# Kernel tuning notes

Measured on AMD Instinct MI355X. Metric: run time of the kernel, lower is better.

The kernel has to match this reference:

```python
import jax, jax.numpy as jnp
import numpy as np

N, IN_C, HID, H1, E, EP = 4096, 256, 128, 4, 131072, 131072
TH, TL, FF = 4, 2, 512  # transformer heads, layers, ffn dim
D = HID  # transformer d_model


def setup_inputs() -> dict:
    key = jax.random.key(0)
    ks = jax.random.split(key, 32)
    s = 0.05
    inp = {
        'features': jax.random.normal(ks[0], (N, IN_C), jnp.float32),
        'src': jax.random.randint(ks[1], (E,), 0, N),
        'dst': jax.random.randint(ks[2], (E,), 0, N),
        'psrc': jax.random.randint(ks[3], (EP,), 0, N),
        'pdst': jax.random.randint(ks[4], (EP,), 0, N),
        # GAT layer 1: in=256 -> heads=4, out=128
        'W1': jax.random.normal(ks[5], (H1 * HID, IN_C), jnp.float32) * s,
        'al1': jax.random.normal(ks[6], (H1, HID), jnp.float32) * s,
        'ar1': jax.random.normal(ks[7], (H1, HID), jnp.float32) * s,
        'b1': jnp.zeros((H1 * HID,), jnp.float32),
        # GAT layer 2: in=512 -> heads=1, out=128
        'W2': jax.random.normal(ks[8], (HID, H1 * HID), jnp.float32) * s,
        'al2': jax.random.normal(ks[9], (1, HID), jnp.float32) * s,
        'ar2': jax.random.normal(ks[10], (1, HID), jnp.float32) * s,
        'b2': jnp.zeros((HID,), jnp.float32),
        # Transformer encoder (TL layers, torch TransformerEncoderLayer post-norm, relu)
        'tw_qkv': jax.random.normal(ks[11], (TL, 3 * D, D), jnp.float32) * s,
        'tb_qkv': jnp.zeros((TL, 3 * D), jnp.float32),
        'tw_o': jax.random.normal(ks[12], (TL, D, D), jnp.float32) * s,
        'tb_o': jnp.zeros((TL, D), jnp.float32),
        'ln1_g': jnp.ones((TL, D), jnp.float32),
        'ln1_b': jnp.zeros((TL, D), jnp.float32),
        'tw_ff1': jax.random.normal(ks[13], (TL, FF, D), jnp.float32) * s,
        'tb_ff1': jnp.zeros((TL, FF), jnp.float32),
        'tw_ff2': jax.random.normal(ks[14], (TL, D, FF), jnp.float32) * s,
        'tb_ff2': jnp.zeros((TL, D), jnp.float32),
        'ln2_g': jnp.ones((TL, D), jnp.float32),
        'ln2_b': jnp.zeros((TL, D), jnp.float32),
        # decoder MLP
        'fc1_w': jax.random.normal(ks[15], (HID, 2 * HID), jnp.float32) * s,
        'fc1_b': jnp.zeros((HID,), jnp.float32),
        'fc2_w': jax.random.normal(ks[16], (1, HID), jnp.float32) * s,
        'fc2_b': jnp.zeros((1,), jnp.float32),
    }
    return inp


def _leaky(x):
    return jnp.where(x > 0, x, 0.2 * x)


def _gat(x, W, al, ar, b, src, dst, n):
    H, F = al.shape
    h = (x @ W.T).reshape(n, H, F)  # [N,H,F]
    el = jnp.sum(h * al[None], -1)  # [N,H]
    er = jnp.sum(h * ar[None], -1)
    e = _leaky(el[src] + er[dst])  # [E,H]
    m = jax.ops.segment_max(e, dst, num_segments=n)
    ex = jnp.exp(e - m[dst])
    ssum = jax.ops.segment_sum(ex, dst, num_segments=n)
    alpha = ex / ssum[dst]  # edge softmax over incoming edges of dst
    out = jax.ops.segment_sum(h[src] * alpha[:, :, None], dst, num_segments=n)
    return out + b.reshape(1, H, F)


def _ln(x, g, b):
    mu = jnp.mean(x, -1, keepdims=True)
    var = jnp.mean((x - mu) ** 2, -1, keepdims=True)
    return (x - mu) / jnp.sqrt(var + 1e-5) * g + b


def _encoder_layer(h, wqkv, bqkv, wo, bo, g1, b1, wf1, bf1, wf2, bf2, g2, b2):
    n, d = h.shape
    hd = d // TH
    qkv = h @ wqkv.T + bqkv
    q, k, v = jnp.split(qkv, 3, axis=-1)
    q = q.reshape(n, TH, hd)
    k = k.reshape(n, TH, hd)
    v = v.reshape(n, TH, hd)
    scores = jnp.einsum('qhd,khd->hqk', q, k) / jnp.sqrt(jnp.float32(hd))
    attn = jax.nn.softmax(scores, axis=-1)
    o = jnp.einsum('hqk,khd->qhd', attn, v).reshape(n, d) @ wo.T + bo
    h = _ln(h + o, g1, b1)
    ff = jax.nn.relu(h @ wf1.T + bf1) @ wf2.T + bf2
    return _ln(h + ff, g2, b2)


def reference(features, W1, al1, ar1, b1, W2, al2, ar2, b2,
              tw_qkv, tb_qkv, tw_o, tb_o, ln1_g, ln1_b,
              tw_ff1, tb_ff1, tw_ff2, tb_ff2, ln2_g, ln2_b,
              fc1_w, fc1_b, fc2_w, fc2_b, src, dst, psrc, pdst):
    n = features.shape[0]
    h = _gat(features, W1, al1, ar1, b1, src, dst, n)  # [N,4,128]
    h = jax.nn.relu(h.reshape(n, -1))                  # [N,512]
    h = _gat(h, W2, al2, ar2, b2, src, dst, n)[:, 0]   # [N,128]
    for i in range(TL):
        h = _encoder_layer(h, tw_qkv[i], tb_qkv[i], tw_o[i], tb_o[i],
                           ln1_g[i], ln1_b[i], tw_ff1[i], tb_ff1[i],
                           tw_ff2[i], tb_ff2[i], ln2_g[i], ln2_b[i])
    ef = jnp.concatenate([h[psrc], h[pdst]], axis=1)   # [EP,256]
    x = jax.nn.relu(ef @ fc1_w.T + fc1_b)
    return jax.nn.sigmoid(x @ fc2_w.T + fc2_b)         # [EP,1]
```

## Files before the change

kernel.cpp:

```cpp
#include <hip/hip_runtime.h>
#include <hip/hip_bf16.h>
#include <math.h>

#define NN   4096
#define INC  256
#define HIDF 128
#define H1H  4
#define DM   128
#define THD  4
#define FFD  512

typedef __attribute__((ext_vector_type(8))) short bf16x8;
typedef __attribute__((ext_vector_type(4))) float f32x4;

__device__ __forceinline__ float leaky(float x){ return x > 0.f ? x : 0.2f*x; }

__device__ __forceinline__ ushort f2b(float f){
  __hip_bfloat16 h = __float2bfloat16(f);
  return __builtin_bit_cast(ushort, h);
}
__device__ __forceinline__ unsigned pk2(float a, float b){
  return (unsigned)f2b(a) | ((unsigned)f2b(b) << 16);
}
__device__ __forceinline__ float b2f(unsigned u){ return __uint_as_float(u << 16); }
__device__ __forceinline__ float b2flo(unsigned u){ return __uint_as_float(u << 16); }
__device__ __forceinline__ float b2fhi(unsigned u){ return __uint_as_float(u & 0xffff0000u); }

__device__ __forceinline__ int kvperm(int kv){
  return (kv & ~31) | ((kv & 12) << 1) | ((kv >> 2) & 4) | (kv & 3);
}

template<bool BIAS, bool RELU, bool OUTBF, bool ABF>
__global__ __launch_bounds__(256) void gemm_mf(
    const void* __restrict__ Av, const ushort* __restrict__ Wb,
    const float* __restrict__ bias, void* __restrict__ Cv,
    int M, int N, int K, int ldw)
{
  __shared__ uint4 As4[512];
  __shared__ uint4 Bs4[512];
  int tid = threadIdx.x;
  int row0 = blockIdx.y * 64, col0 = blockIdx.x * 64;
  int wid = tid >> 6, lane = tid & 63;
  int wm = wid >> 1, wn = wid & 1;
  int ql = lane & 15, g = lane >> 4;
  const f32x4 z4 = {0.f,0.f,0.f,0.f};
  f32x4 acc[2][2] = {z4,z4,z4,z4};

  for (int k0 = 0; k0 < K; k0 += 64) {
    #pragma unroll
    for (int p = 0; p < 2; p++) {
      int idx = tid + p*256;
      int ko = idx & 7, mm = idx >> 3;
      if constexpr (ABF) {
        As4[ko*64 + mm] = *(const uint4*)((const ushort*)Av + (size_t)(row0 + mm)*K + k0 + ko*8);
      } else {
        const float* sa = (const float*)Av + (size_t)(row0 + mm)*K + k0 + ko*8;
        float4 a0 = *(const float4*)sa;
        float4 a1 = *(const float4*)(sa + 4);
        uint4 av;
        av.x = pk2(a0.x, a0.y); av.y = pk2(a0.z, a0.w);
        av.z = pk2(a1.x, a1.y); av.w = pk2(a1.z, a1.w);
        As4[ko*64 + mm] = av;
      }
      Bs4[ko*64 + mm] = *(const uint4*)(Wb + (size_t)(col0 + mm)*ldw + k0 + ko*8);
    }
    __syncthreads();
    #pragma unroll
    for (int kk = 0; kk < 2; kk++) {
      int ko = kk*4 + g;
      bf16x8 a0 = *((const bf16x8*)As4 + ko*64 + wm*32 + ql);
      bf16x8 a1 = *((const bf16x8*)As4 + ko*64 + wm*32 + 16 + ql);
      bf16x8 b0 = *((const bf16x8*)Bs4 + ko*64 + wn*32 + ql);
      bf16x8 b1 = *((const bf16x8*)Bs4 + ko*64 + wn*32 + 16 + ql);
      acc[0][0] = __builtin_amdgcn_mfma_f32_16x16x32_bf16(a0, b0, acc[0][0], 0,0,0);
      acc[0][1] = __builtin_amdgcn_mfma_f32_16x16x32_bf16(a0, b1, acc[0][1], 0,0,0);
      acc[1][0] = __builtin_amdgcn_mfma_f32_16x16x32_bf16(a1, b0, acc[1][0], 0,0,0);
      acc[1][1] = __builtin_amdgcn_mfma_f32_16x16x32_bf16(a1, b1, acc[1][1], 0,0,0);
    }
    __syncthreads();
  }
  float bvs[2] = {0.f, 0.f};
  if (BIAS) {
    bvs[0] = bias[col0 + wn*32 + ql];
    bvs[1] = bias[col0 + wn*32 + 16 + ql];
  }
  #pragma unroll
  for (int fm = 0; fm < 2; fm++)
    #pragma unroll
    for (int fn = 0; fn < 2; fn++) {
      int row = row0 + wm*32 + fm*16 + g*4;
      int col = col0 + wn*32 + fn*16 + ql;
      #pragma unroll
      for (int r = 0; r < 4; r++) {
        float v = acc[fm][fn][r];
        if (BIAS) v += bvs[fn];
        if (RELU) v = fmaxf(v, 0.f);
        if (OUTBF) ((ushort*)Cv)[(size_t)(row + r)*N + col] = f2b(v);
        else       ((float*)Cv)[(size_t)(row + r)*N + col] = v;
      }
    }
}

__global__ __launch_bounds__(256) void gemm_qkv(
    const ushort* __restrict__ Ab, const ushort* __restrict__ Wb,
    const float* __restrict__ bias,
    ushort* __restrict__ qb, ushort* __restrict__ kt, ushort* __restrict__ vt)
{
  __shared__ uint4 As4[512];
  __shared__ uint4 Bs4[512];
  int tid = threadIdx.x;
  int row0 = blockIdx.y * 64, col0 = blockIdx.x * 64;
  int wid = tid >> 6, lane = tid & 63;
  int wm = wid >> 1, wn = wid & 1;
  int ql = lane & 15, g = lane >> 4;
  const f32x4 z4 = {0.f,0.f,0.f,0.f};
  f32x4 acc[2][2] = {z4,z4,z4,z4};

  for (int k0 = 0; k0 < 128; k0 += 64) {
    #pragma unroll
    for (int p = 0; p < 2; p++) {
      int idx = tid + p*256;
      int ko = idx & 7, mm = idx >> 3;
      As4[ko*64 + mm] = *(const uint4*)(Ab + (size_t)(row0 + mm)*128 + k0 + ko*8);
      Bs4[ko*64 + mm] = *(const uint4*)(Wb + (size_t)(col0 + mm)*128 + k0 + ko*8);
    }
    __syncthreads();
    #pragma unroll
    for (int kk = 0; kk < 2; kk++) {
      int ko = kk*4 + g;
      bf16x8 a0 = *((const bf16x8*)As4 + ko*64 + wm*32 + ql);
      bf16x8 a1 = *((const bf16x8*)As4 + ko*64 + wm*32 + 16 + ql);
      bf16x8 b0 = *((const bf16x8*)Bs4 + ko*64 + wn*32 + ql);
      bf16x8 b1 = *((const bf16x8*)Bs4 + ko*64 + wn*32 + 16 + ql);
      acc[0][0] = __builtin_amdgcn_mfma_f32_16x16x32_bf16(a0, b0, acc[0][0], 0,0,0);
      acc[0][1] = __builtin_amdgcn_mfma_f32_16x16x32_bf16(a0, b1, acc[0][1], 0,0,0);
      acc[1][0] = __builtin_amdgcn_mfma_f32_16x16x32_bf16(a1, b0, acc[1][0], 0,0,0);
      acc[1][1] = __builtin_amdgcn_mfma_f32_16x16x32_bf16(a1, b1, acc[1][1], 0,0,0);
    }
    __syncthreads();
  }
  float bvs[2];
  bvs[0] = bias[col0 + wn*32 + ql];
  bvs[1] = bias[col0 + wn*32 + 16 + ql];
  #pragma unroll
  for (int fm = 0; fm < 2; fm++)
    #pragma unroll
    for (int fn = 0; fn < 2; fn++) {
      int row = row0 + wm*32 + fm*16 + g*4;
      int col = col0 + wn*32 + fn*16 + ql;
      #pragma unroll
      for (int r = 0; r < 4; r++) {
        float v = acc[fm][fn][r] + bvs[fn];
        int kv = row + r;
        if (col < 128) {
          qb[(size_t)kv*128 + col] = f2b(v * 0.25505654708f);
        } else if (col < 256) {
          int hh = (col - 128) >> 5, d = (col - 128) & 31;
          kt[(size_t)hh*131072 + (size_t)kv*32 + d] = f2b(v);
        } else {
          int hh = (col - 256) >> 5, d = (col - 256) & 31;
          vt[(size_t)hh*131072 + (size_t)(kv >> 5)*1024 + (d >> 4)*512
             + (d & 15)*32 + kvperm(kv & 31)] = f2b(v);
        }
      }
    }
}

__global__ __launch_bounds__(256) void gemm_ln(
    const ushort* __restrict__ Ab, const ushort* __restrict__ Wb,
    const float* __restrict__ bias, ushort* __restrict__ h,
    const float* __restrict__ lng, const float* __restrict__ lnb, int K)
{
  __shared__ uint4 As4[128];
  __shared__ uint4 Bs4[1024];
  __shared__ float xs[16][132];
  int tid = threadIdx.x;
  int row0 = blockIdx.x * 16;
  int wv = tid >> 6, lane = tid & 63;
  int ql = lane & 15, g = lane >> 4;
  const f32x4 z4 = {0.f,0.f,0.f,0.f};
  f32x4 acc[2] = {z4, z4};

  for (int k0 = 0; k0 < K; k0 += 64) {
    if (tid < 128) {
      int ko = tid & 7, mm = tid >> 3;
      As4[ko*16 + mm] = *(const uint4*)(Ab + (size_t)(row0 + mm)*K + k0 + ko*8);
    }
    #pragma unroll
    for (int p = 0; p < 4; p++) {
      int idx = tid + p*256;
      int ko = idx & 7, nn = idx >> 3;
      Bs4[ko*128 + nn] = *(const uint4*)(Wb + (size_t)nn*K + k0 + ko*8);
    }
    __syncthreads();
    #pragma unroll
    for (int kk = 0; kk < 2; kk++) {
      int ko = kk*4 + g;
      bf16x8 a = *((const bf16x8*)As4 + ko*16 + ql);
      #pragma unroll
      for (int fn = 0; fn < 2; fn++) {
        bf16x8 b = *((const bf16x8*)Bs4 + ko*128 + wv*32 + fn*16 + ql);
        acc[fn] = __builtin_amdgcn_mfma_f32_16x16x32_bf16(a, b, acc[fn], 0,0,0);
      }
    }
    __syncthreads();
  }
  #pragma unroll
  for (int fn = 0; fn < 2; fn++) {
    int col = wv*32 + fn*16 + ql;
    float bv = bias[col];
    #pragma unroll
    for (int r = 0; r < 4; r++) xs[g*4 + r][col] = acc[fn][r] + bv;
  }
  __syncthreads();
  int rl = tid >> 4, cl = tid & 15, c0 = cl * 8;
  ushort* hrow = h + (size_t)(row0 + rl)*128;
  uint4 rv = *(const uint4*)(hrow + c0);
  float x[8];
  x[0] = xs[rl][c0+0] + b2flo(rv.x); x[1] = xs[rl][c0+1] + b2fhi(rv.x);
  x[2] = xs[rl][c0+2] + b2flo(rv.y); x[3] = xs[rl][c0+3] + b2fhi(rv.y);
  x[4] = xs[rl][c0+4] + b2flo(rv.z); x[5] = xs[rl][c0+5] + b2fhi(rv.z);
  x[6] = xs[rl][c0+6] + b2flo(rv.w); x[7] = xs[rl][c0+7] + b2fhi(rv.w);
  float s1 = 0.f, s2 = 0.f;
  #pragma unroll
  for (int i = 0; i < 8; i++) { s1 += x[i]; s2 += x[i]*x[i]; }
  #pragma unroll
  for (int st = 1; st < 16; st <<= 1) {
    s1 += __shfl_xor(s1, st); s2 += __shfl_xor(s2, st);
  }
  float mean = s1 * (1.f/128.f);
  float var  = s2 * (1.f/128.f) - mean*mean;
  float rstd = rsqrtf(var + 1e-5f);
  float o[8];
  #pragma unroll
  for (int i = 0; i < 8; i += 4) {
    float4 g4 = *(const float4*)(lng + c0 + i);
    float4 b4 = *(const float4*)(lnb + c0 + i);
    o[i+0] = (x[i+0]-mean)*rstd*g4.x + b4.x;
    o[i+1] = (x[i+1]-mean)*rstd*g4.y + b4.y;
    o[i+2] = (x[i+2]-mean)*rstd*g4.z + b4.z;
    o[i+3] = (x[i+3]-mean)*rstd*g4.w + b4.w;
  }
  uint4 ov; ov.x = pk2(o[0],o[1]); ov.y = pk2(o[2],o[3]);
  ov.z = pk2(o[4],o[5]); ov.w = pk2(o[6],o[7]);
  *(uint4*)(hrow + c0) = ov;
}

__global__ __launch_bounds__(256) void cvt_weights(
    const float* __restrict__ W1, const float* __restrict__ W2,
    const float* __restrict__ qkv, const float* __restrict__ o,
    const float* __restrict__ ff1, const float* __restrict__ ff2,
    const float* __restrict__ fc1, const float* __restrict__ fc1b,
    ushort* __restrict__ out, float* __restrict__ bias256)
{
  if (blockIdx.x == 608) {
    int t = threadIdx.x;
    bias256[t] = (t < 128) ? fc1b[t] : 0.f;
    return;
  }
  int i4 = (blockIdx.x*256 + threadIdx.x) * 4;
  const float* s; int loc;
  size_t dst = i4;
  if      (i4 < 131072) { s = W1;  loc = i4; }
  else if (i4 < 196608) { s = W2;  loc = i4 - 131072; }
  else if (i4 < 294912) { s = qkv; loc = i4 - 196608; }
  else if (i4 < 327680) { s = o;   loc = i4 - 294912; }
  else if (i4 < 458752) { s = ff1; loc = i4 - 327680; }
  else if (i4 < 589824) { s = ff2; loc = i4 - 458752; }
  else {
    s = fc1; loc = i4 - 589824;
    int j = loc >> 8, k2 = loc & 255;
    dst = 589824 + ((k2 >= 128) ? 16384 : 0) + j*128 + (k2 & 127);
  }
  float4 v = *(const float4*)(s + loc);
  uint2 w; w.x = pk2(v.x, v.y); w.y = pk2(v.z, v.w);
  *(uint2*)(out + dst) = w;
}

__global__ __launch_bounds__(256) void cvt_feat(
    const float* __restrict__ f, ushort* __restrict__ o)
{
  int i = (blockIdx.x * 256 + threadIdx.x) * 4;
  float4 v = *(const float4*)(f + i);
  uint2 w; w.x = pk2(v.x, v.y); w.y = pk2(v.z, v.w);
  *(uint2*)(o + i) = w;
}

__global__ void count_kernel(const int* __restrict__ dst, int* __restrict__ deg, int E) {
  int e = blockIdx.x * blockDim.x + threadIdx.x;
  if (e < E) atomicAdd(&deg[dst[e]], 1);
}
__global__ __launch_bounds__(1024) void scan_kernel(
    const int* __restrict__ deg, int* __restrict__ rowstart, int* __restrict__ cursor)
{
  __shared__ int sdata[1024];
  int t = threadIdx.x;
  int base = t * 4;
  int v0 = deg[base], v1 = deg[base+1], v2 = deg[base+2], v3 = deg[base+3];
  int tot = v0 + v1 + v2 + v3;
  sdata[t] = tot;
  __syncthreads();
  for (int off = 1; off < 1024; off <<= 1) {
    int x = (t >= off) ? sdata[t - off] : 0;
    __syncthreads();
    sdata[t] += x;
    __syncthreads();
  }
  int run = sdata[t] - tot;
  rowstart[base]   = run; cursor[base]   = run; run += v0;
  rowstart[base+1] = run; cursor[base+1] = run; run += v1;
  rowstart[base+2] = run; cursor[base+2] = run; run += v2;
  rowstart[base+3] = run; cursor[base+3] = run; run += v3;
  if (t == 1023) rowstart[4096] = run;
}
__global__ void fill_kernel(const int* __restrict__ src, const int* __restrict__ dst,
                            int* __restrict__ cursor, int* __restrict__ nbr, int E) {
  int e = blockIdx.x * blockDim.x + threadIdx.x;
  if (e < E) {
    int p = atomicAdd(&cursor[dst[e]], 1);
    nbr[p] = src[e];
  }
}

template<int H>
__global__ __launch_bounds__(256) void elr_kernel(
    const ushort* __restrict__ hmat, const float* __restrict__ al,
    const float* __restrict__ ar, float* __restrict__ el, float* __restrict__ er)
{
  int w = threadIdx.x >> 6, lane = threadIdx.x & 63;
  int n = blockIdx.x * 4 + w;
  if constexpr (H == 4) {
    int hh = lane >> 4, f0 = (lane & 15) * 8;
    bf16x8 hv = *(const bf16x8*)(hmat + (size_t)n*512 + hh*128 + f0);
    float4 a0 = *(const float4*)(al + hh*128 + f0);
    float4 a1 = *(const float4*)(al + hh*128 + f0 + 4);
    float4 r0 = *(const float4*)(ar + hh*128 + f0);
    float4 r1 = *(const float4*)(ar + hh*128 + f0 + 4);
    float x[8];
    #pragma unroll
    for (int i = 0; i < 8; i++) x[i] = b2f((ushort)hv[i]);
    float e1 = x[0]*a0.x + x[1]*a0.y + x[2]*a0.z + x[3]*a0.w
             + x[4]*a1.x + x[5]*a1.y + x[6]*a1.z + x[7]*a1.w;
    float e2 = x[0]*r0.x + x[1]*r0.y + x[2]*r0.z + x[3]*r0.w
             + x[4]*r1.x + x[5]*r1.y + x[6]*r1.z + x[7]*r1.w;
    #pragma unroll
    for (int s = 1; s < 16; s <<= 1) { e1 += __shfl_xor(e1, s); e2 += __shfl_xor(e2, s); }
    if ((lane & 15) == 0) { el[n*4 + hh] = e1; er[n*4 + hh] = e2; }
  } else {
    int f0 = lane * 2;
    unsigned u = *(const unsigned*)(hmat + (size_t)n*128 + f0);
    float x0 = b2flo(u), x1 = b2fhi(u);
    float2 av = *(const float2*)(al + f0);
    float2 rv = *(const float2*)(ar + f0);
    float e1 = x0*av.x + x1*av.y;
    float e2 = x0*rv.x + x1*rv.y;
    #pragma unroll
    for (int s = 1; s < 64; s <<= 1) { e1 += __shfl_xor(e1, s); e2 += __shfl_xor(e2, s); }
    if (lane == 0) { el[n] = e1; er[n] = e2; }
  }
}

__global__ __launch_bounds__(256) void gat_agg4(
    const ushort* __restrict__ hsrc, const float* __restrict__ el, const float* __restrict__ er,
    const int* __restrict__ rowstart, const int* __restrict__ nbr,
    const float* __restrict__ bias, ushort* __restrict__ out)
{
  __shared__ float s_alpha[4][256][4];
  __shared__ int   s_nbr[4][256];
  int wv = threadIdx.x >> 6, lane = threadIdx.x & 63;
  int n = blockIdx.x * 4 + wv;
  int e0 = rowstart[n];
  int deg = rowstart[n+1] - e0;
  float4 ern = *(const float4*)(er + (size_t)n*4);
  int hh = lane >> 4;
  float acc[8] = {};
  if (deg > 0 && deg <= 256) {
    float se0=0.f, se1=0.f, se2=0.f, se3=0.f;
    for (int i = lane; i < deg; i += 64) {
      int s = nbr[e0 + i];
      s_nbr[wv][i] = s;
      float4 ev = *(const float4*)(el + (size_t)s*4);
      float p0 = __expf(leaky(ev.x + ern.x));
      float p1 = __expf(leaky(ev.y + ern.y));
      float p2 = __expf(leaky(ev.z + ern.z));
      float p3 = __expf(leaky(ev.w + ern.w));
      s_alpha[wv][i][0] = p0; s_alpha[wv][i][1] = p1;
      s_alpha[wv][i][2] = p2; s_alpha[wv][i][3] = p3;
      se0 += p0; se1 += p1; se2 += p2; se3 += p3;
    }
    #pragma unroll
    for (int st = 1; st < 64; st <<= 1) {
      se0 += __shfl_xor(se0, st); se1 += __shfl_xor(se1, st);
      se2 += __shfl_xor(se2, st); se3 += __shfl_xor(se3, st);
    }
    float si = 1.f / ((hh == 0) ? se0 : (hh == 1) ? se1 : (hh == 2) ? se2 : se3);
    #pragma unroll 4
    for (int i = 0; i < deg; i++) {
      float a = s_alpha[wv][i][hh] * si;
      int s = s_nbr[wv][i];
      uint4 hv = *(const uint4*)(hsrc + (size_t)s*512 + lane*8);
      acc[0] += a * b2flo(hv.x); acc[1] += a * b2fhi(hv.x);
      acc[2] += a * b2flo(hv.y); acc[3] += a * b2fhi(hv.y);
      acc[4] += a * b2flo(hv.z); acc[5] += a * b2fhi(hv.z);
      acc[6] += a * b2flo(hv.w); acc[7] += a * b2fhi(hv.w);
    }
  } else if (deg > 0) {
    float se0=0.f, se1=0.f, se2=0.f, se3=0.f;
    for (int i = lane; i < deg; i += 64) {
      int s = nbr[e0 + i];
      float4 ev = *(const float4*)(el + (size_t)s*4);
      se0 += __expf(leaky(ev.x + ern.x));
      se1 += __expf(leaky(ev.y + ern.y));
      se2 += __expf(leaky(ev.z + ern.z));
      se3 += __expf(leaky(ev.w + ern.w));
    }
    #pragma unroll
    for (int st = 1; st < 64; st <<= 1) {
      se0 += __shfl_xor(se0, st); se1 += __shfl_xor(se1, st);
      se2 += __shfl_xor(se2, st); se3 += __shfl_xor(se3, st);
    }
    float si0 = 1.f/se0, si1 = 1.f/se1, si2 = 1.f/se2, si3 = 1.f/se3;
    for (int c = 0; c < deg; c += 256) {
      int cn = min(256, deg - c);
      for (int i = lane; i < cn; i += 64) {
        int s = nbr[e0 + c + i];
        s_nbr[wv][i] = s;
        float4 ev = *(const float4*)(el + (size_t)s*4);
        s_alpha[wv][i][0] = __expf(leaky(ev.x + ern.x)) * si0;
        s_alpha[wv][i][1] = __expf(leaky(ev.y + ern.y)) * si1;
        s_alpha[wv][i][2] = __expf(leaky(ev.z + ern.z)) * si2;
        s_alpha[wv][i][3] = __expf(leaky(ev.w + ern.w)) * si3;
      }
      #pragma unroll 4
      for (int i = 0; i < cn; i++) {
        float a = s_alpha[wv][i][hh];
        int s = s_nbr[wv][i];
        uint4 hv = *(const uint4*)(hsrc + (size_t)s*512 + lane*8);
        acc[0] += a * b2flo(hv.x); acc[1] += a * b2fhi(hv.x);
        acc[2] += a * b2flo(hv.y); acc[3] += a * b2fhi(hv.y);
        acc[4] += a * b2flo(hv.z); acc[5] += a * b2fhi(hv.z);
        acc[6] += a * b2flo(hv.w); acc[7] += a * b2fhi(hv.w);
      }
    }
  }
  const float* bp = bias + lane*8;
  float4 b0 = *(const float4*)(bp);
  float4 b1 = *(const float4*)(bp + 4);
  float v0 = fmaxf(acc[0]+b0.x, 0.f), v1 = fmaxf(acc[1]+b0.y, 0.f);
  float v2 = fmaxf(acc[2]+b0.z, 0.f), v3 = fmaxf(acc[3]+b0.w, 0.f);
  float v4 = fmaxf(acc[4]+b1.x, 0.f), v5 = fmaxf(acc[5]+b1.y, 0.f);
  float v6 = fmaxf(acc[6]+b1.z, 0.f), v7 = fmaxf(acc[7]+b1.w, 0.f);
  uint4 ov; ov.x = pk2(v0,v1); ov.y = pk2(v2,v3); ov.z = pk2(v4,v5); ov.w = pk2(v6,v7);
  *(uint4*)(out + (size_t)n*512 + lane*8) = ov;
}

__global__ __launch_bounds__(256) void gat_agg1(
    const ushort* __restrict__ hsrc, const float* __restrict__ el, const float* __restrict__ er,
    const int* __restrict__ rowstart, const int* __restrict__ nbr,
    const float* __restrict__ bias, ushort* __restrict__ out)
{
  __shared__ float s_alpha[4][256];
  __shared__ int   s_nbr[4][256];
  int wv = threadIdx.x >> 6, lane = threadIdx.x & 63;
  int n = blockIdx.x * 4 + wv;
  int e0 = rowstart[n];
  int deg = rowstart[n+1] - e0;
  float ern = er[n];
  float a0 = 0.f, a1 = 0.f;
  if (deg > 0 && deg <= 256) {
    float se = 0.f;
    for (int i = lane; i < deg; i += 64) {
      int s = nbr[e0 + i];
      s_nbr[wv][i] = s;
      float p = __expf(leaky(el[s] + ern));
      s_alpha[wv][i] = p;
      se += p;
    }
    #pragma unroll
    for (int st = 1; st < 64; st <<= 1) se += __shfl_xor(se, st);
    float si = 1.f / se;
    #pragma unroll 4
    for (int i = 0; i < deg; i++) {
      float a = s_alpha[wv][i] * si;
      int s = s_nbr[wv][i];
      unsigned u = *(const unsigned*)(hsrc + (size_t)s*128 + lane*2);
      a0 += a * b2flo(u);
      a1 += a * b2fhi(u);
    }
  } else if (deg > 0) {
    float se = 0.f;
    for (int i = lane; i < deg; i += 64)
      se += __expf(leaky(el[nbr[e0 + i]] + ern));
    #pragma unroll
    for (int st = 1; st < 64; st <<= 1) se += __shfl_xor(se, st);
    float si = 1.f / se;
    for (int c = 0; c < deg; c += 256) {
      int cn = min(256, deg - c);
      for (int i = lane; i < cn; i += 64) {
        int s = nbr[e0 + c + i];
        s_nbr[wv][i] = s;
        s_alpha[wv][i] = __expf(leaky(el[s] + ern)) * si;
      }
      #pragma unroll 4
      for (int i = 0; i < cn; i++) {
        float a = s_alpha[wv][i];
        int s = s_nbr[wv][i];
        unsigned u = *(const unsigned*)(hsrc + (size_t)s*128 + lane*2);
        a0 += a * b2flo(u);
        a1 += a * b2fhi(u);
      }
    }
  }
  float v0 = a0 + bias[lane*2], v1 = a1 + bias[lane*2 + 1];
  *(unsigned*)(out + (size_t)n*128 + lane*2) = pk2(v0, v1);
}

#define LOADFRAGS(KF, VF, KV)                                              \
  {                                                                        \
    int _kv = (KV);                                                        \
    if (_kv < 512) {                                                       \
      const ushort* _kp = kptr + (size_t)_kv * 32;                         \
      const ushort* _vp = vptr + (size_t)_kv * 32;                         \
      KF[0] = *(const bf16x8*)(_kp);                                       \
      KF[1] = *(const bf16x8*)(_kp + 512);                                 \
      KF[2] = *(const bf16x8*)(_kp + 1024);                                \
      KF[3] = *(const bf16x8*)(_kp + 1536);                                \
      VF[0] = *(const bf16x8*)(_vp);                                       \
      VF[1] = *(const bf16x8*)(_vp + 1024);                                \
      VF[2] = *(const bf16x8*)(_vp + 512);                                 \
      VF[3] = *(const bf16x8*)(_vp + 1536);                                \
    }                                                                      \
  }

#define QPASS(QF, LS, OA, OB, KF, VF)                                      \
  {                                                                        \
    f32x4 st0 = __builtin_amdgcn_mfma_f32_16x16x32_bf16(KF[0], QF, z4, 0, 0, 0); \
    f32x4 st1 = __builtin_amdgcn_mfma_f32_16x16x32_bf16(KF[1], QF, z4, 0, 0, 0); \
    f32x4 st2 = __builtin_amdgcn_mfma_f32_16x16x32_bf16(KF[2], QF, z4, 0, 0, 0); \
    f32x4 st3 = __builtin_amdgcn_mfma_f32_16x16x32_bf16(KF[3], QF, z4, 0, 0, 0); \
    float pvv[16];                                                         \
    _Pragma("unroll")                                                      \
    for (int i = 0; i < 4; i++) {                                          \
      pvv[i] = st0[i]; pvv[4+i] = st1[i]; pvv[8+i] = st2[i]; pvv[12+i] = st3[i]; \
    }                                                                      \
    _Pragma("unroll")                                                      \
    for (int i = 0; i < 16; i++) { pvv[i] = exp2f(pvv[i]); LS += pvv[i]; } \
    bf16x8 pf0 = { (short)f2b(pvv[0]),  (short)f2b(pvv[1]),  (short)f2b(pvv[2]),  (short)f2b(pvv[3]),   \
                   (short)f2b(pvv[4]),  (short)f2b(pvv[5]),  (short)f2b(pvv[6]),  (short)f2b(pvv[7]) }; \
    bf16x8 pf1 = { (short)f2b(pvv[8]),  (short)f2b(pvv[9]),  (short)f2b(pvv[10]), (short)f2b(pvv[11]),  \
                   (short)f2b(pvv[12]), (short)f2b(pvv[13]), (short)f2b(pvv[14]), (short)f2b(pvv[15]) };\
    OA = __builtin_amdgcn_mfma_f32_16x16x32_bf16(VF[0], pf0, OA, 0, 0, 0); \
    OA = __builtin_amdgcn_mfma_f32_16x16x32_bf16(VF[1], pf1, OA, 0, 0, 0); \
    OB = __builtin_amdgcn_mfma_f32_16x16x32_bf16(VF[2], pf0, OB, 0, 0, 0); \
    OB = __builtin_amdgcn_mfma_f32_16x16x32_bf16(VF[3], pf1, OB, 0, 0, 0); \
  }

#define ATTN_BODY(KF, VF, KN, VN, KV)                                      \
  {                                                                        \
    LOADFRAGS(KN, VN, (KV) + 64);                                          \
    QPASS(qf0, ls0, o00, o01, KF, VF);                                     \
    QPASS(qf1, ls1, o10, o11, KF, VF);                                     \
  }

__global__ __launch_bounds__(512) void attn_mfma(
    const ushort* __restrict__ qb,
    const ushort* __restrict__ kt,
    const ushort* __restrict__ vt,
    ushort* __restrict__ attnout)
{
  int lane = threadIdx.x & 63;
  int w    = threadIdx.x >> 6;
  int head = blockIdx.x >> 7;
  int q0   = (blockIdx.x & 127) * 32;
  int ql = lane & 15;
  int g  = lane >> 4;
  const f32x4 z4 = {0.f, 0.f, 0.f, 0.f};
  int kvbase = w * 512;

  bf16x8 qf0 = *(const bf16x8*)(qb + (size_t)(q0 + ql)*128      + head*32 + g*8);
  bf16x8 qf1 = *(const bf16x8*)(qb + (size_t)(q0 + 16 + ql)*128 + head*32 + g*8);
  const ushort* kptr = kt + (size_t)head*131072 + (size_t)kvbase*32 + ql*32 + g*8;
  const ushort* vptr = vt + (size_t)head*131072 + (size_t)kvbase*32 + ql*32 + g*8;

  float ls0 = 0.f, ls1 = 0.f;
  f32x4 o00 = z4, o01 = z4, o10 = z4, o11 = z4;

  bf16x8 kfA[4], vfA[4], kfB[4], vfB[4];
  LOADFRAGS(kfA, vfA, 0);
  for (int kv0 = 0; kv0 < 512; kv0 += 128) {
    ATTN_BODY(kfA, vfA, kfB, vfB, kv0);
    ATTN_BODY(kfB, vfB, kfA, vfA, kv0 + 64);
  }

  ls0 += __shfl_xor(ls0, 16); ls0 += __shfl_xor(ls0, 32);
  ls1 += __shfl_xor(ls1, 16); ls1 += __shfl_xor(ls1, 32);

  __shared__ float so[8][32][36];
  __shared__ float sl[8][32];
  if (g == 0) { sl[w][ql] = ls0; sl[w][16 + ql] = ls1; }
  #pragma unroll
  for (int r = 0; r < 4; r++) {
    so[w][ql][g*4 + r]           = o00[r];
    so[w][ql][16 + g*4 + r]      = o01[r];
    so[w][16 + ql][g*4 + r]      = o10[r];
    so[w][16 + ql][16 + g*4 + r] = o11[r];
  }
  __syncthreads();
  int q  = threadIdx.x >> 4;
  int d0 = (threadIdx.x & 15) * 2;
  float L = 0.f, O0 = 0.f, O1 = 0.f;
  #pragma unroll
  for (int w2 = 0; w2 < 8; w2++) {
    L  += sl[w2][q];
    O0 += so[w2][q][d0];
    O1 += so[w2][q][d0+1];
  }
  float rl = 1.f / L;
  *(unsigned*)(attnout + (size_t)(q0 + q)*128 + head*32 + d0) = pk2(O0*rl, O1*rl);
}

__global__ __launch_bounds__(256) void pair_kernel(
    const ushort* __restrict__ ABp,
    const int* __restrict__ ps, const int* __restrict__ pd,
    const float* __restrict__ fc2w, const float* __restrict__ fc2b,
    float* __restrict__ out, int EP)
{
  int gw = (blockIdx.x * blockDim.x + threadIdx.x) >> 6;
  int lane = threadIdx.x & 63;
  int nw = (gridDim.x * blockDim.x) >> 6;
  float w0 = fc2w[2*lane], w1 = fc2w[2*lane + 1];
  float bb = fc2b[0];
  for (int p = gw*2; p < EP; p += nw*2) {
    int sA = ps[p], dA = pd[p];
    bool hasB = (p + 1 < EP);
    int sB = hasB ? ps[p+1] : sA;
    int dB = hasB ? pd[p+1] : dA;
    unsigned avA = *(const unsigned*)(ABp + (size_t)sA*256 + 2*lane);
    unsigned bvA = *(const unsigned*)(ABp + (size_t)dA*256 + 128 + 2*lane);
    unsigned avB = *(const unsigned*)(ABp + (size_t)sB*256 + 2*lane);
    unsigned bvB = *(const unsigned*)(ABp + (size_t)dB*256 + 128 + 2*lane);
    float accA = fmaxf(b2flo(avA) + b2flo(bvA), 0.f)*w0
               + fmaxf(b2fhi(avA) + b2fhi(bvA), 0.f)*w1;
    float accB = fmaxf(b2flo(avB) + b2flo(bvB), 0.f)*w0
               + fmaxf(b2fhi(avB) + b2fhi(bvB), 0.f)*w1;
    #pragma unroll
    for (int off = 32; off > 0; off >>= 1) {
      accA += __shfl_down(accA, off);
      accB += __shfl_down(accB, off);
    }
    if (lane == 0) {
      out[p] = 1.f / (1.f + __expf(-(accA + bb)));
      if (hasB) out[p+1] = 1.f / (1.f + __expf(-(accB + bb)));
    }
  }
}

extern "C" void kernel_launch(void* const* d_in, const int* in_sizes, int n_in,
                              void* d_out, int out_size, void* d_ws, size_t ws_size,
                              hipStream_t stream)
{
  const float* features = (const float*)d_in[0];
  const int*   src      = (const int*)d_in[1];
  const int*   dst      = (const int*)d_in[2];
  const int*   psrc     = (const int*)d_in[3];
  const int*   pdst     = (const int*)d_in[4];
  const float* W1   = (const float*)d_in[5];
  const float* al1  = (const float*)d_in[6];
  const float* ar1  = (const float*)d_in[7];
  const float* b1   = (const float*)d_in[8];
  const float* W2   = (const float*)d_in[9];
  const float* al2  = (const float*)d_in[10];
  const float* ar2  = (const float*)d_in[11];
  const float* b2   = (const float*)d_in[12];
  const float* tw_qkv = (const float*)d_in[13];
  const float* tb_qkv = (const float*)d_in[14];
  const float* tw_o   = (const float*)d_in[15];
  const float* tb_o   = (const float*)d_in[16];
  const float* ln1_g  = (const float*)d_in[17];
  const float* ln1_b  = (const float*)d_in[18];
  const float* tw_ff1 = (const float*)d_in[19];
  const float* tb_ff1 = (const float*)d_in[20];
  const float* tw_ff2 = (const float*)d_in[21];
  const float* tb_ff2 = (const float*)d_in[22];
  const float* ln2_g  = (const float*)d_in[23];
  const float* ln2_b  = (const float*)d_in[24];
  const float* fc1_w  = (const float*)d_in[25];
  const float* fc1_b  = (const float*)d_in[26];
  const float* fc2_w  = (const float*)d_in[27];
  const float* fc2_b  = (const float*)d_in[28];
  int E  = in_sizes[1];
  int EP = in_sizes[3];

  float* ws = (float*)d_ws;
  size_t off = 0;
  auto alloc = [&](size_t n) { float* p = ws + off; off += n; return p; };
  ushort* hb    = (ushort*)alloc((size_t)NN * 64);
  ushort* featb = (ushort*)alloc((size_t)NN * 128);
  ushort* h1b   = (ushort*)alloc((size_t)NN * 256);
  ushort* h2b   = (ushort*)alloc((size_t)NN * 256);
  ushort* bigb  = (ushort*)alloc((size_t)NN * 256);
  ushort* hgb   = (ushort*)alloc((size_t)NN * 64);
  ushort* qb    = (ushort*)alloc((size_t)NN * 64);
  ushort* attnb = (ushort*)alloc((size_t)NN * 64);
  ushort* kt    = (ushort*)alloc((size_t)NN * 64);
  ushort* vt    = (ushort*)alloc((size_t)NN * 64);
  ushort* wbf   = (ushort*)alloc(622592/2);
  ushort* ABp   = (ushort*)alloc((size_t)NN * 128);
  float*  bias256 = alloc(256);
  float*  el1   = alloc((size_t)NN * 4);
  float*  er1   = alloc((size_t)NN * 4);
  float*  el2   = alloc((size_t)NN);
  float*  er2   = alloc((size_t)NN);
  int* ibase    = (int*)(ws + off);
  int* deg      = ibase;
  int* rowstart = ibase + 4096;
  int* cursor   = rowstart + 4097;
  int* nbr      = cursor + 4096;

  const size_t oW1 = 0, oW2 = 131072, oQKV = 196608, oO = 294912,
               oFF1 = 327680, oFF2 = 458752, oFC1 = 589824;

  cvt_weights<<<609, 256, 0, stream>>>(W1, W2, tw_qkv, tw_o, tw_ff1, tw_ff2,
                                       fc1_w, fc1_b, wbf, bias256);
  cvt_feat<<<1024, 256, 0, stream>>>(features, featb);

  hipMemsetAsync(deg, 0, 4096 * sizeof(int), stream);
  count_kernel<<<(E + 255)/256, 256, 0, stream>>>(dst, deg, E);
  scan_kernel<<<1, 1024, 0, stream>>>(deg, rowstart, cursor);
  fill_kernel<<<(E + 255)/256, 256, 0, stream>>>(src, dst, cursor, nbr, E);

  gemm_mf<false,false,true,true><<<dim3(8, 64), 256, 0, stream>>>(
      featb, wbf + oW1, nullptr, h1b, NN, 512, 256, 256);
  elr_kernel<4><<<1024, 256, 0, stream>>>(h1b, al1, ar1, el1, er1);
  gat_agg4<<<1024, 256, 0, stream>>>(h1b, el1, er1, rowstart, nbr, b1, h2b);

  gemm_mf<false,false,true,true><<<dim3(2, 64), 256, 0, stream>>>(
      h2b, wbf + oW2, nullptr, hgb, NN, 128, 512, 512);
  elr_kernel<1><<<1024, 256, 0, stream>>>(hgb, al2, ar2, el2, er2);
  gat_agg1<<<1024, 256, 0, stream>>>(hgb, el2, er2, rowstart, nbr, b2, hb);

  for (int l = 0; l < 2; l++) {
    gemm_qkv<<<dim3(6, 64), 256, 0, stream>>>(
        hb, wbf + oQKV + (size_t)l*49152, tb_qkv + l*384, qb, kt, vt);
    attn_mfma<<<512, 512, 0, stream>>>(qb, kt, vt, attnb);
    gemm_ln<<<256, 256, 0, stream>>>(
        attnb, wbf + oO + (size_t)l*16384, tb_o + l*128, hb,
        ln1_g + l*128, ln1_b + l*128, 128);
    gemm_mf<true,true,true,true><<<dim3(8, 64), 256, 0, stream>>>(
        hb, wbf + oFF1 + (size_t)l*65536, tb_ff1 + l*512, bigb, NN, 512, 128, 128);
    gemm_ln<<<256, 256, 0, stream>>>(
        bigb, wbf + oFF2 + (size_t)l*65536, tb_ff2 + l*128, hb,
        ln2_g + l*128, ln2_b + l*128, 512);
  }

  gemm_mf<true,false,true,true><<<dim3(4, 64), 256, 0, stream>>>(
      hb, wbf + oFC1, bias256, ABp, NN, 256, 128, 128);
  pair_kernel<<<1024, 256, 0, stream>>>(ABp, psrc, pdst, fc2_w, fc2_b, (float*)d_out, EP);
}
```

Before: 212.4 us.

## Fuse layer-2 GAT projection with attention logits; merge conversion kernels; widen pair batching

Adds a dedicated GEMM kernel for the second GAT projection that also computes the el/er attention logits in its epilogue from fp32 accumulators, removing a separate elr launch and a reread of the projected features. The weight and feature bf16 conversion kernels are merged into one launch. The pair decoder kernel now processes four pairs per wave iteration instead of two, to raise memory-level parallelism on the gathers. In exchange, the new GEMM uses 16-row tiles and reloads the full 128x64 weight tile per block, and el/er now come from fp32 values rather than bf16-rounded ones.

```diff
diff --git a/kernel.cpp b/kernel.cpp
--- a/kernel.cpp
+++ b/kernel.cpp
@@ -246,19 +246,97 @@
   *(uint4*)(hrow + c0) = ov;
 }
 
-__global__ __launch_bounds__(256) void cvt_weights(
+__global__ __launch_bounds__(256) void gemm_hg_elr(
+    const ushort* __restrict__ Ab, const ushort* __restrict__ Wb,
+    const float* __restrict__ al, const float* __restrict__ ar,
+    ushort* __restrict__ hg, float* __restrict__ el, float* __restrict__ er)
+{
+  __shared__ uint4 As4[128];
+  __shared__ uint4 Bs4[1024];
+  __shared__ float xs[16][132];
+  int tid = threadIdx.x;
+  int row0 = blockIdx.x * 16;
+  int wv = tid >> 6, lane = tid & 63;
+  int ql = lane & 15, g = lane >> 4;
+  const f32x4 z4 = {0.f,0.f,0.f,0.f};
+  f32x4 acc[2] = {z4, z4};
+
+  for (int k0 = 0; k0 < 512; k0 += 64) {
+    if (tid < 128) {
+      int ko = tid & 7, mm = tid >> 3;
+      As4[ko*16 + mm] = *(const uint4*)(Ab + (size_t)(row0 + mm)*512 + k0 + ko*8);
+    }
+    #pragma unroll
+    for (int p = 0; p < 4; p++) {
+      int idx = tid + p*256;
+      int ko = idx & 7, nn = idx >> 3;
+      Bs4[ko*128 + nn] = *(const uint4*)(Wb + (size_t)nn*512 + k0 + ko*8);
+    }
+    __syncthreads();
+    #pragma unroll
+    for (int kk = 0; kk < 2; kk++) {
+      int ko = kk*4 + g;
+      bf16x8 a = *((const bf16x8*)As4 + ko*16 + ql);
+      #pragma unroll
+      for (int fn = 0; fn < 2; fn++) {
+        bf16x8 b = *((const bf16x8*)Bs4 + ko*128 + wv*32 + fn*16 + ql);
+        acc[fn] = __builtin_amdgcn_mfma_f32_16x16x32_bf16(a, b, acc[fn], 0,0,0);
+      }
+    }
+    __syncthreads();
+  }
+  #pragma unroll
+  for (int fn = 0; fn < 2; fn++) {
+    int col = wv*32 + fn*16 + ql;
+    #pragma unroll
+    for (int r = 0; r < 4; r++) xs[g*4 + r][col] = acc[fn][r];
+  }
+  __syncthreads();
+  int rl = tid >> 4, cl = tid & 15, c0 = cl * 8;
+  float e1 = 0.f, e2 = 0.f;
+  float x[8];
+  #pragma unroll
+  for (int i = 0; i < 8; i += 4) {
+    float4 a4 = *(const float4*)(al + c0 + i);
+    float4 r4 = *(const float4*)(ar + c0 + i);
+    x[i+0] = xs[rl][c0+i+0]; x[i+1] = xs[rl][c0+i+1];
+    x[i+2] = xs[rl][c0+i+2]; x[i+3] = xs[rl][c0+i+3];
+    e1 += x[i+0]*a4.x + x[i+1]*a4.y + x[i+2]*a4.z + x[i+3]*a4.w;
+    e2 += x[i+0]*r4.x + x[i+1]*r4.y + x[i+2]*r4.z + x[i+3]*r4.w;
+  }
+  uint4 ov; ov.x = pk2(x[0],x[1]); ov.y = pk2(x[2],x[3]);
+  ov.z = pk2(x[4],x[5]); ov.w = pk2(x[6],x[7]);
+  *(uint4*)(hg + (size_t)(row0 + rl)*128 + c0) = ov;
+  #pragma unroll
+  for (int st = 1; st < 16; st <<= 1) {
+    e1 += __shfl_xor(e1, st); e2 += __shfl_xor(e2, st);
+  }
+  if (cl == 0) { el[row0 + rl] = e1; er[row0 + rl] = e2; }
+}
+
+__global__ __launch_bounds__(256) void cvt_all(
     const float* __restrict__ W1, const float* __restrict__ W2,
     const float* __restrict__ qkv, const float* __restrict__ o,
     const float* __restrict__ ff1, const float* __restrict__ ff2,
     const float* __restrict__ fc1, const float* __restrict__ fc1b,
-    ushort* __restrict__ out, float* __restrict__ bias256)
-{
-  if (blockIdx.x == 608) {
+    const float* __restrict__ feat,
+    ushort* __restrict__ out, float* __restrict__ bias256,
+    ushort* __restrict__ featb)
+{
+  int b = blockIdx.x;
+  if (b == 608) {
     int t = threadIdx.x;
     bias256[t] = (t < 128) ? fc1b[t] : 0.f;
     return;
   }
-  int i4 = (blockIdx.x*256 + threadIdx.x) * 4;
+  if (b >= 609) {
+    int i = ((b - 609)*256 + threadIdx.x) * 4;
+    float4 v = *(const float4*)(feat + i);
+    uint2 w; w.x = pk2(v.x, v.y); w.y = pk2(v.z, v.w);
+    *(uint2*)(featb + i) = w;
+    return;
+  }
+  int i4 = (b*256 + threadIdx.x) * 4;
   const float* s; int loc;
   size_t dst = i4;
   if      (i4 < 131072) { s = W1;  loc = i4; }
@@ -277,15 +355,6 @@
   *(uint2*)(out + dst) = w;
 }
 
-__global__ __launch_bounds__(256) void cvt_feat(
-    const float* __restrict__ f, ushort* __restrict__ o)
-{
-  int i = (blockIdx.x * 256 + threadIdx.x) * 4;
-  float4 v = *(const float4*)(f + i);
-  uint2 w; w.x = pk2(v.x, v.y); w.y = pk2(v.z, v.w);
-  *(uint2*)(o + i) = w;
-}
-
 __global__ void count_kernel(const int* __restrict__ dst, int* __restrict__ deg, int E) {
   int e = blockIdx.x * blockDim.x + threadIdx.x;
   if (e < E) atomicAdd(&deg[dst[e]], 1);
@@ -322,42 +391,28 @@
   }
 }
 
-template<int H>
-__global__ __launch_bounds__(256) void elr_kernel(
+__global__ __launch_bounds__(256) void elr4_kernel(
     const ushort* __restrict__ hmat, const float* __restrict__ al,
     const float* __restrict__ ar, float* __restrict__ el, float* __restrict__ er)
 {
   int w = threadIdx.x >> 6, lane = threadIdx.x & 63;
   int n = blockIdx.x * 4 + w;
-  if constexpr (H == 4) {
-    int hh = lane >> 4, f0 = (lane & 15) * 8;
-    bf16x8 hv = *(const bf16x8*)(hmat + (size_t)n*512 + hh*128 + f0);
-    float4 a0 = *(const float4*)(al + hh*128 + f0);
-    float4 a1 = *(const float4*)(al + hh*128 + f0 + 4);
-    float4 r0 = *(const float4*)(ar + hh*128 + f0);
-    float4 r1 = *(const float4*)(ar + hh*128 + f0 + 4);
-    float x[8];
-    #pragma unroll
-    for (int i = 0; i < 8; i++) x[i] = b2f((ushort)hv[i]);
-    float e1 = x[0]*a0.x + x[1]*a0.y + x[2]*a0.z + x[3]*a0.w
-             + x[4]*a1.x + x[5]*a1.y + x[6]*a1.z + x[7]*a1.w;
-    float e2 = x[0]*r0.x + x[1]*r0.y + x[2]*r0.z + x[3]*r0.w
-             + x[4]*r1.x + x[5]*r1.y + x[6]*r1.z + x[7]*r1.w;
-    #pragma unroll
-    for (int s = 1; s < 16; s <<= 1) { e1 += __shfl_xor(e1, s); e2 += __shfl_xor(e2, s); }
-    if ((lane & 15) == 0) { el[n*4 + hh] = e1; er[n*4 + hh] = e2; }
-  } else {
-    int f0 = lane * 2;
-    unsigned u = *(const unsigned*)(hmat + (size_t)n*128 + f0);
-    float x0 = b2flo(u), x1 = b2fhi(u);
-    float2 av = *(const float2*)(al + f0);
-    float2 rv = *(const float2*)(ar + f0);
-    float e1 = x0*av.x + x1*av.y;
-    float e2 = x0*rv.x + x1*rv.y;
-    #pragma unroll
-    for (int s = 1; s < 64; s <<= 1) { e1 += __shfl_xor(e1, s); e2 += __shfl_xor(e2, s); }
-    if (lane == 0) { el[n] = e1; er[n] = e2; }
-  }
+  int hh = lane >> 4, f0 = (lane & 15) * 8;
+  bf16x8 hv = *(const bf16x8*)(hmat + (size_t)n*512 + hh*128 + f0);
+  float4 a0 = *(const float4*)(al + hh*128 + f0);
+  float4 a1 = *(const float4*)(al + hh*128 + f0 + 4);
+  float4 r0 = *(const float4*)(ar + hh*128 + f0);
+  float4 r1 = *(const float4*)(ar + hh*128 + f0 + 4);
+  float x[8];
+  #pragma unroll
+  for (int i = 0; i < 8; i++) x[i] = b2f((ushort)hv[i]);
+  float e1 = x[0]*a0.x + x[1]*a0.y + x[2]*a0.z + x[3]*a0.w
+           + x[4]*a1.x + x[5]*a1.y + x[6]*a1.z + x[7]*a1.w;
+  float e2 = x[0]*r0.x + x[1]*r0.y + x[2]*r0.z + x[3]*r0.w
+           + x[4]*r1.x + x[5]*r1.y + x[6]*r1.z + x[7]*r1.w;
+  #pragma unroll
+  for (int s = 1; s < 16; s <<= 1) { e1 += __shfl_xor(e1, s); e2 += __shfl_xor(e2, s); }
+  if ((lane & 15) == 0) { el[n*4 + hh] = e1; er[n*4 + hh] = e2; }
 }
 
 __global__ __launch_bounds__(256) void gat_agg4(
@@ -630,27 +685,26 @@
   int nw = (gridDim.x * blockDim.x) >> 6;
   float w0 = fc2w[2*lane], w1 = fc2w[2*lane + 1];
   float bb = fc2b[0];
-  for (int p = gw*2; p < EP; p += nw*2) {
-    int sA = ps[p], dA = pd[p];
-    bool hasB = (p + 1 < EP);
-    int sB = hasB ? ps[p+1] : sA;
-    int dB = hasB ? pd[p+1] : dA;
-    unsigned avA = *(const unsigned*)(ABp + (size_t)sA*256 + 2*lane);
-    unsigned bvA = *(const unsigned*)(ABp + (size_t)dA*256 + 128 + 2*lane);
-    unsigned avB = *(const unsigned*)(ABp + (size_t)sB*256 + 2*lane);
-    unsigned bvB = *(const unsigned*)(ABp + (size_t)dB*256 + 128 + 2*lane);
-    float accA = fmaxf(b2flo(avA) + b2flo(bvA), 0.f)*w0
-               + fmaxf(b2fhi(avA) + b2fhi(bvA), 0.f)*w1;
-    float accB = fmaxf(b2flo(avB) + b2flo(bvB), 0.f)*w0
-               + fmaxf(b2fhi(avB) + b2fhi(bvB), 0.f)*w1;
+  for (int p = gw*4; p < EP; p += nw*4) {
+    float acc[4];
+    #pragma unroll
+    for (int k = 0; k < 4; k++) {
+      int pp = (p + k < EP) ? (p + k) : (EP - 1);
+      int s = ps[pp], d = pd[pp];
+      unsigned av = *(const unsigned*)(ABp + (size_t)s*256 + 2*lane);
+      unsigned bv = *(const unsigned*)(ABp + (size_t)d*256 + 128 + 2*lane);
+      acc[k] = fmaxf(b2flo(av) + b2flo(bv), 0.f)*w0
+             + fmaxf(b2fhi(av) + b2fhi(bv), 0.f)*w1;
+    }
     #pragma unroll
     for (int off = 32; off > 0; off >>= 1) {
-      accA += __shfl_down(accA, off);
-      accB += __shfl_down(accB, off);
+      #pragma unroll
+      for (int k = 0; k < 4; k++) acc[k] += __shfl_down(acc[k], off);
     }
     if (lane == 0) {
-      out[p] = 1.f / (1.f + __expf(-(accA + bb)));
-      if (hasB) out[p+1] = 1.f / (1.f + __expf(-(accB + bb)));
+      #pragma unroll
+      for (int k = 0; k < 4; k++)
+        if (p + k < EP) out[p + k] = 1.f / (1.f + __expf(-(acc[k] + bb)));
     }
   }
 }
@@ -720,9 +774,8 @@
   const size_t oW1 = 0, oW2 = 131072, oQKV = 196608, oO = 294912,
                oFF1 = 327680, oFF2 = 458752, oFC1 = 589824;
 
-  cvt_weights<<<609, 256, 0, stream>>>(W1, W2, tw_qkv, tw_o, tw_ff1, tw_ff2,
-                                       fc1_w, fc1_b, wbf, bias256);
-  cvt_feat<<<1024, 256, 0, stream>>>(features, featb);
+  cvt_all<<<1633, 256, 0, stream>>>(W1, W2, tw_qkv, tw_o, tw_ff1, tw_ff2,
+                                    fc1_w, fc1_b, features, wbf, bias256, featb);
 
   hipMemsetAsync(deg, 0, 4096 * sizeof(int), stream);
   count_kernel<<<(E + 255)/256, 256, 0, stream>>>(dst, deg, E);
@@ -731,12 +784,10 @@
 
   gemm_mf<false,false,true,true><<<dim3(8, 64), 256, 0, stream>>>(
       featb, wbf + oW1, nullptr, h1b, NN, 512, 256, 256);
-  elr_kernel<4><<<1024, 256, 0, stream>>>(h1b, al1, ar1, el1, er1);
+  elr4_kernel<<<1024, 256, 0, stream>>>(h1b, al1, ar1, el1, er1);
   gat_agg4<<<1024, 256, 0, stream>>>(h1b, el1, er1, rowstart, nbr, b1, h2b);
 
-  gemm_mf<false,false,true,true><<<dim3(2, 64), 256, 0, stream>>>(
-      h2b, wbf + oW2, nullptr, hgb, NN, 128, 512, 512);
-  elr_kernel<1><<<1024, 256, 0, stream>>>(hgb, al2, ar2, el2, er2);
+  gemm_hg_elr<<<256, 256, 0, stream>>>(h2b, wbf + oW2, al2, ar2, hgb, el2, er2);
   gat_agg1<<<1024, 256, 0, stream>>>(hgb, el2, er2, rowstart, nbr, b2, hb);
 
   for (int l = 0; l < 2; l++) {
```

After: 200.4 us. 5.6% less time.
